# Performance work log

Measured on AMD Instinct MI355X. Metric: run time of the kernel, lower is better.

Reference implementation:

```python
import jax, jax.numpy as jnp
import numpy as np

EPS = 1e-6
ROLL = jnp.array([1, 2, 3, 0])  # next-vertex index for box edges
MAX_VERT = 9  # 8 polygon vertices max + 1 closing duplicate


def box2corners(box):
    # box: [B,N,5] = (x, y, w, h, alpha) -> corners [B,N,4,2]
    x, y, w, h, a = jnp.split(box, 5, axis=-1)  # each [B,N,1]
    x4 = jnp.array([0.5, -0.5, -0.5, 0.5], box.dtype) * w  # [B,N,4]
    y4 = jnp.array([0.5, 0.5, -0.5, -0.5], box.dtype) * h
    corners = jnp.stack([x4, y4], axis=-1)                 # [B,N,4,2]
    sin, cos = jnp.sin(a), jnp.cos(a)
    rot_T = jnp.stack([jnp.concatenate([cos, sin], -1),
                       jnp.concatenate([-sin, cos], -1)], axis=-2)  # [B,N,2,2]
    rotated = jnp.einsum('bnvc,bncd->bnvd', corners, rot_T)
    return rotated + jnp.stack([x, y], axis=-1)            # broadcast [B,N,1,2]


def box_intersection(c1, c2):
    # all-pairs edge/edge intersection of the two quads
    line1 = jnp.concatenate([c1, c1[:, :, ROLL, :]], axis=3)  # [B,N,4,4]
    line2 = jnp.concatenate([c2, c2[:, :, ROLL, :]], axis=3)
    l1 = line1[:, :, :, None, :]  # [B,N,4,1,4]
    l2 = line2[:, :, None, :, :]  # [B,N,1,4,4]
    x1, y1, x2, y2 = (l1[..., i] for i in range(4))
    x3, y3, x4, y4 = (l2[..., i] for i in range(4))
    num = (x1 - x2) * (y3 - y4) - (y1 - y2) * (x3 - x4)
    den_t = (x1 - x3) * (y3 - y4) - (y1 - y3) * (x3 - x4)
    t = den_t / num
    mask_t = (t >= 0) & (t <= 1)
    den_u = (x1 - x2) * (y1 - y3) - (y1 - y2) * (x1 - x3)
    u = -den_u / num
    mask_u = (u >= 0) & (u <= 1)
    mask = mask_t & mask_u                                  # [B,N,4,4]
    t = den_t / (num + EPS)
    pts = jnp.stack([x1 + t * (x2 - x1), y1 + t * (y2 - y1)], axis=-1)
    pts = pts * mask[..., None].astype(pts.dtype)           # [B,N,4,4,2]
    return pts, mask


def box1_in_box2(c1, c2):
    # ray-casting point-in-polygon for each corner of box1 against box2
    rel = c2[:, :, None, :, :] - c1[:, :, :, None, :]       # [B,N,4,4,2]
    x, y = rel[..., 0], rel[..., 1]
    lx, ly = x[..., ROLL], y[..., ROLL]
    m1 = (ly > 0) ^ (y > 0)
    m2 = x - y * (lx - x) / (ly - y) > 0
    return jnp.sum((m1 & m2).astype(jnp.int32), axis=-1) % 2 == 1  # [B,N,4]


def sort_indices(vertices, mask):
    # JAX equivalent of the custom diff_iou_rotated_sort_vertices kernel:
    # sort valid vertices CCW by angle about the valid-mean, pad with the
    # first valid index (duplicates contribute zero shoelace area).
    nv = jnp.sum(mask, axis=2).astype(jnp.int32)            # [B,N]
    mf = mask[..., None].astype(vertices.dtype)
    mean = jnp.sum(vertices * mf, axis=2, keepdims=True) / \
        jnp.maximum(nv, 1)[..., None, None].astype(vertices.dtype)
    vn = vertices - mean
    ang = jnp.arctan2(vn[..., 1], vn[..., 0])               # [B,N,24]
    ang = jnp.where(mask, ang, jnp.inf)                     # invalid -> end
    order = jnp.argsort(ang, axis=-1)
    cand = order[..., :MAX_VERT]                            # [B,N,9]
    first = cand[..., :1]
    pos = jnp.arange(MAX_VERT)
    return jnp.where(pos < nv[..., None], cand, first)      # int32 [B,N,9]


def calc_area(idx_sorted, vertices):
    idx = jnp.broadcast_to(idx_sorted[..., None], idx_sorted.shape + (2,))
    sel = jnp.take_along_axis(vertices, idx, axis=2)        # [B,N,9,2]
    total = sel[:, :, :-1, 0] * sel[:, :, 1:, 1] - \
            sel[:, :, :-1, 1] * sel[:, :, 1:, 0]
    return jnp.abs(jnp.sum(total, axis=2)) / 2              # [B,N]


def _forward(box1, box2):
    c1 = box2corners(box1)
    c2 = box2corners(box2)
    B, N = c1.shape[0], c1.shape[1]
    inters, valid = box_intersection(c1, c2)
    c12 = box1_in_box2(c1, c2)
    c21 = box1_in_box2(c2, c1)
    vertices = jnp.concatenate([c1, c2, inters.reshape(B, N, -1, 2)], axis=2)  # [B,N,24,2]
    mask = jnp.concatenate([c12, c21, valid.reshape(B, N, -1)], axis=2)        # [B,N,24]
    idx = sort_indices(vertices, mask)
    intersection = calc_area(idx, vertices)
    area1 = box1[:, :, 2] * box1[:, :, 3]
    area2 = box2[:, :, 2] * box2[:, :, 3]
    union = area1 + area2 - intersection
    return intersection / union


def setup_inputs() -> dict:
    key = jax.random.key(0)
    k1, k2, k3, k4, k5, k6 = jax.random.split(key, 6)
    B, N = 4, 131072
    ctr = jax.random.uniform(k1, (B, N, 2), minval=-10.0, maxval=10.0)
    wh1 = jax.random.uniform(k2, (B, N, 2), minval=1.0, maxval=4.0)
    a1 = jax.random.uniform(k3, (B, N, 1), minval=0.0, maxval=float(np.pi))
    box1 = jnp.concatenate([ctr, wh1, a1], axis=-1)
    ctr2 = ctr + jax.random.uniform(k4, (B, N, 2), minval=-1.0, maxval=1.0)
    wh2 = jax.random.uniform(k5, (B, N, 2), minval=1.0, maxval=4.0)
    a2 = jax.random.uniform(k6, (B, N, 1), minval=0.0, maxval=float(np.pi))
    box2 = jnp.concatenate([ctr2, wh2, a2], axis=-1)
    return {"box1": box1, "box2": box2}


def reference(box1, box2):
    return _forward(box1, box2)
```

## Files before the change

### kernel.cpp

```cpp
#include <hip/hip_runtime.h>
#include <math.h>

#define TPB 256

__device__ __forceinline__ float frcp(float x) {
#if __has_builtin(__builtin_amdgcn_rcpf)
    return __builtin_amdgcn_rcpf(x);
#else
    return 1.0f / x;
#endif
}

#define INV_2PI 0.15915494309189535f
__device__ __forceinline__ float fsin(float a) {
#if __has_builtin(__builtin_amdgcn_sinf)
    return __builtin_amdgcn_sinf(a * INV_2PI);
#else
    return sinf(a);
#endif
}
__device__ __forceinline__ float fcos(float a) {
#if __has_builtin(__builtin_amdgcn_cosf)
    return __builtin_amdgcn_cosf(a * INV_2PI);
#else
    return cosf(a);
#endif
}

__device__ __forceinline__ float fclamp(float x, float lo, float hi) {
    return fminf(fmaxf(x, lo), hi);
}

__global__ __launch_bounds__(TPB, 8) void diff_iou_rotated_kernel(
    const float* __restrict__ box1, const float* __restrict__ box2,
    float* __restrict__ out, int n)
{
    const int g = blockIdx.x * TPB + threadIdx.x;
    if (g >= n) return;

    const float* p1 = box1 + (size_t)g * 5;
    const float* p2 = box2 + (size_t)g * 5;
    const float cx1 = p1[0], cy1 = p1[1], w1 = p1[2], h1 = p1[3], a1 = p1[4];
    const float cx2 = p2[0], cy2 = p2[1], w2 = p2[2], h2 = p2[3], a2 = p2[4];

    const float s1a = fsin(a1), c1a = fcos(a1);
    const float s2a = fsin(a2), c2a = fcos(a2);

    const float W = 0.5f * w1, H = 0.5f * h1;
    const float sumarea = w1 * h1 + w2 * h2;

    const float dxc = cx2 - cx1, dyc = cy2 - cy1;
    const float lx =  c1a * dxc + s1a * dyc;
    const float ly = -s1a * dxc + c1a * dyc;
    const float cr = c2a * c1a + s2a * s1a;
    const float sr = s2a * c1a - c2a * s1a;

    const float sxc[4] = {0.5f, -0.5f, -0.5f, 0.5f};
    const float syc[4] = {0.5f, 0.5f, -0.5f, -0.5f};
    float vx[4], vy[4];
    #pragma unroll
    for (int i = 0; i < 4; ++i) {
        const float ox = sxc[i] * w2, oy = syc[i] * h2;
        vx[i] = ox * cr - oy * sr + lx;
        vy[i] = ox * sr + oy * cr + ly;
    }

    float acc = 0.0f;
    #pragma unroll
    for (int i = 0; i < 4; ++i) {
        const float px = vx[i],           py = vy[i];
        const float qx = vx[(i + 1) & 3], qy = vy[(i + 1) & 3];
        const float dx = qx - px, dy = qy - py;
        const float dys = (dy == 0.0f) ? 1e-30f : dy;
        const float dxs = (dx == 0.0f) ? 1e-30f : dx;

        const float r  = frcp(dys);
        const float t0 = (-H - py) * r;
        const float t1 = ( H - py) * r;
        const float ta = fclamp(fminf(t0, t1), 0.0f, 1.0f);
        const float tb = fclamp(fmaxf(t0, t1), 0.0f, 1.0f);

        const float rx = frcp(dxs);
        const float s0 = (-W - px) * rx;
        const float s1 = ( W - px) * rx;
        const float sa = fclamp(fminf(s0, s1), ta, tb);
        const float sb = fclamp(fmaxf(s0, s1), ta, tb);

        const float ya  = fmaf(ta, dy, py);
        const float ysa = fmaf(sa, dy, py);
        const float ysb = fmaf(sb, dy, py);
        const float yb  = fmaf(tb, dy, py);

        const float xac = fclamp(fmaf(ta, dx, px), -W, W);
        const float xbc = fclamp(fmaf(tb, dx, px), -W, W);
        const float xm  = fmaf(0.5f * (sa + sb), dx, px);

        acc = fmaf(xac, ysa - ya, acc);
        acc = fmaf(xm,  ysb - ysa, acc);
        acc = fmaf(xbc, yb - ysb, acc);
    }

    const float inter = fabsf(acc);
    out[g] = inter * frcp(sumarea - inter);
}

extern "C" void kernel_launch(void* const* d_in, const int* in_sizes, int n_in,
                              void* d_out, int out_size, void* d_ws, size_t ws_size,
                              hipStream_t stream) {
    const float* b1 = (const float*)d_in[0];
    const float* b2 = (const float*)d_in[1];
    float* out = (float*)d_out;
    const int n = in_sizes[0] / 5;
    const int blocks = (n + TPB - 1) / TPB;
    hipLaunchKernelGGL(diff_iou_rotated_kernel, dim3(blocks), dim3(TPB), 0, stream,
                       b1, b2, out, n);
}
```

Measured before the change: 9.914 us.

## Process two boxes per thread with float2 loads and shared edge reciprocals

```diff
diff --git a/kernel.cpp b/kernel.cpp
--- a/kernel.cpp
+++ b/kernel.cpp
@@ -31,23 +31,36 @@
     return fminf(fmaxf(x, lo), hi);
 }
 
-__global__ __launch_bounds__(TPB, 8) void diff_iou_rotated_kernel(
-    const float* __restrict__ box1, const float* __restrict__ box2,
-    float* __restrict__ out, int n)
-{
-    const int g = blockIdx.x * TPB + threadIdx.x;
-    if (g >= n) return;
+__device__ __forceinline__ float edge_int(float px, float py, float dx, float dy,
+                                          float rx, float ry, float W, float H) {
+    const float t0 = (-H - py) * ry;
+    const float t1 = ( H - py) * ry;
+    const float ta = fclamp(fminf(t0, t1), 0.0f, 1.0f);
+    const float tb = fclamp(fmaxf(t0, t1), 0.0f, 1.0f);
 
-    const float* p1 = box1 + (size_t)g * 5;
-    const float* p2 = box2 + (size_t)g * 5;
-    const float cx1 = p1[0], cy1 = p1[1], w1 = p1[2], h1 = p1[3], a1 = p1[4];
-    const float cx2 = p2[0], cy2 = p2[1], w2 = p2[2], h2 = p2[3], a2 = p2[4];
+    const float s0 = (-W - px) * rx;
+    const float s1 = ( W - px) * rx;
+    const float sa = fclamp(fminf(s0, s1), ta, tb);
+    const float sb = fclamp(fmaxf(s0, s1), ta, tb);
 
+    const float ya  = fmaf(ta, dy, py);
+    const float ysa = fmaf(sa, dy, py);
+    const float ysb = fmaf(sb, dy, py);
+    const float yb  = fmaf(tb, dy, py);
+
+    const float xac = fclamp(fmaf(ta, dx, px), -W, W);
+    const float xbc = fclamp(fmaf(tb, dx, px), -W, W);
+    const float xm  = fmaf(0.5f * (sa + sb), dx, px);
+
+    return xac * (ysa - ya) + xm * (ysb - ysa) + xbc * (yb - ysb);
+}
+
+__device__ __forceinline__ float iou_pair(float cx1, float cy1, float w1, float h1, float a1,
+                                          float cx2, float cy2, float w2, float h2, float a2) {
     const float s1a = fsin(a1), c1a = fcos(a1);
     const float s2a = fsin(a2), c2a = fcos(a2);
 
     const float W = 0.5f * w1, H = 0.5f * h1;
-    const float sumarea = w1 * h1 + w2 * h2;
 
     const float dxc = cx2 - cx1, dyc = cy2 - cy1;
     const float lx =  c1a * dxc + s1a * dyc;
@@ -55,53 +68,56 @@
     const float cr = c2a * c1a + s2a * s1a;
     const float sr = s2a * c1a - c2a * s1a;
 
-    const float sxc[4] = {0.5f, -0.5f, -0.5f, 0.5f};
-    const float syc[4] = {0.5f, 0.5f, -0.5f, -0.5f};
-    float vx[4], vy[4];
-    #pragma unroll
-    for (int i = 0; i < 4; ++i) {
-        const float ox = sxc[i] * w2, oy = syc[i] * h2;
-        vx[i] = ox * cr - oy * sr + lx;
-        vy[i] = ox * sr + oy * cr + ly;
-    }
+    const float ux = w2 * cr, uy = w2 * sr;
+    const float vx = -h2 * sr, vy = h2 * cr;
+    const float hux = 0.5f * ux, huy = 0.5f * uy;
+    const float hvx = 0.5f * vx, hvy = 0.5f * vy;
+    const float c0x = lx + hux + hvx, c0y = ly + huy + hvy;
+    const float c1x = lx - hux + hvx, c1y = ly - huy + hvy;
+    const float c2x = lx - hux - hvx, c2y = ly - huy - hvy;
+    const float c3x = lx + hux - hvx, c3y = ly + huy - hvy;
 
-    float acc = 0.0f;
-    #pragma unroll
-    for (int i = 0; i < 4; ++i) {
-        const float px = vx[i],           py = vy[i];
-        const float qx = vx[(i + 1) & 3], qy = vy[(i + 1) & 3];
-        const float dx = qx - px, dy = qy - py;
-        const float dys = (dy == 0.0f) ? 1e-30f : dy;
-        const float dxs = (dx == 0.0f) ? 1e-30f : dx;
+    const float rux = frcp(ux == 0.0f ? 1e-30f : ux);
+    const float ruy = frcp(uy == 0.0f ? 1e-30f : uy);
+    const float rvx = frcp(vx == 0.0f ? 1e-30f : vx);
+    const float rvy = frcp(vy == 0.0f ? 1e-30f : vy);
 
-        const float r  = frcp(dys);
-        const float t0 = (-H - py) * r;
-        const float t1 = ( H - py) * r;
-        const float ta = fclamp(fminf(t0, t1), 0.0f, 1.0f);
-        const float tb = fclamp(fmaxf(t0, t1), 0.0f, 1.0f);
-
-        const float rx = frcp(dxs);
-        const float s0 = (-W - px) * rx;
-        const float s1 = ( W - px) * rx;
-        const float sa = fclamp(fminf(s0, s1), ta, tb);
-        const float sb = fclamp(fmaxf(s0, s1), ta, tb);
-
-        const float ya  = fmaf(ta, dy, py);
-        const float ysa = fmaf(sa, dy, py);
-        const float ysb = fmaf(sb, dy, py);
-        const float yb  = fmaf(tb, dy, py);
-
-        const float xac = fclamp(fmaf(ta, dx, px), -W, W);
-        const float xbc = fclamp(fmaf(tb, dx, px), -W, W);
-        const float xm  = fmaf(0.5f * (sa + sb), dx, px);
-
-        acc = fmaf(xac, ysa - ya, acc);
-        acc = fmaf(xm,  ysb - ysa, acc);
-        acc = fmaf(xbc, yb - ysb, acc);
-    }
+    float acc;
+    acc  = edge_int(c0x, c0y, -ux, -uy, -rux, -ruy, W, H);
+    acc += edge_int(c1x, c1y, -vx, -vy, -rvx, -rvy, W, H);
+    acc += edge_int(c2x, c2y,  ux,  uy,  rux,  ruy, W, H);
+    acc += edge_int(c3x, c3y,  vx,  vy,  rvx,  rvy, W, H);
 
     const float inter = fabsf(acc);
-    out[g] = inter * frcp(sumarea - inter);
+    const float sumarea = w1 * h1 + w2 * h2;
+    return inter * frcp(sumarea - inter);
+}
+
+__global__ __launch_bounds__(TPB, 8) void diff_iou_rotated_kernel(
+    const float* __restrict__ box1, const float* __restrict__ box2,
+    float* __restrict__ out, int n)
+{
+    const int t = blockIdx.x * TPB + threadIdx.x;
+    const int i0 = 2 * t;
+    if (i0 >= n) return;
+
+    if (i0 + 1 < n) {
+        const float2* p1 = (const float2*)(box1 + (size_t)i0 * 5);
+        const float2* p2 = (const float2*)(box2 + (size_t)i0 * 5);
+        const float2 A0 = p1[0], A1 = p1[1], A2 = p1[2], A3 = p1[3], A4 = p1[4];
+        const float2 B0 = p2[0], B1 = p2[1], B2 = p2[2], B3 = p2[3], B4 = p2[4];
+
+        const float r0 = iou_pair(A0.x, A0.y, A1.x, A1.y, A2.x,
+                                  B0.x, B0.y, B1.x, B1.y, B2.x);
+        const float r1 = iou_pair(A2.y, A3.x, A3.y, A4.x, A4.y,
+                                  B2.y, B3.x, B3.y, B4.x, B4.y);
+        *(float2*)(out + i0) = make_float2(r0, r1);
+    } else {
+        const float* p1 = box1 + (size_t)i0 * 5;
+        const float* p2 = box2 + (size_t)i0 * 5;
+        out[i0] = iou_pair(p1[0], p1[1], p1[2], p1[3], p1[4],
+                           p2[0], p2[1], p2[2], p2[3], p2[4]);
+    }
 }
 
 extern "C" void kernel_launch(void* const* d_in, const int* in_sizes, int n_in,
@@ -111,7 +127,8 @@
     const float* b2 = (const float*)d_in[1];
     float* out = (float*)d_out;
     const int n = in_sizes[0] / 5;
-    const int blocks = (n + TPB - 1) / TPB;
+    const int nthreads = (n + 1) / 2;
+    const int blocks = (nthreads + TPB - 1) / TPB;
     hipLaunchKernelGGL(diff_iou_rotated_kernel, dim3(blocks), dim3(TPB), 0, stream,
                        b1, b2, out, n);
 }
```

New measurement: 9.722 us. About the same (-1.9%).
